# Performance work log

Hardware: AMD Instinct MI355X
Metric: run time of the kernel (lower is better)

The kernel has to match this reference:

```python
import jax, jax.numpy as jnp
import numpy as np

# Model dims (match init_kwargs)
V, D, NH, H, NL = 32000, 512, 8, 2048, 2
B = 8
SOS = 1
EPS = 1e-5  # PyTorch LayerNorm default
TEMP = 0.8


def _pe(length, d):
    # Sinusoidal positional encoding, same math as PositionalEncoding
    pos = jnp.arange(length, dtype=jnp.float32)[:, None]
    div = jnp.exp(jnp.arange(0, d, 2, dtype=jnp.float32) * (-np.log(10000.0) / d))
    pe = jnp.zeros((length, d), dtype=jnp.float32)
    pe = pe.at[:, 0::2].set(jnp.sin(pos * div))
    pe = pe.at[:, 1::2].set(jnp.cos(pos * div))
    return pe


def _ln(x, g, b):
    m = jnp.mean(x, -1, keepdims=True)
    v = jnp.mean((x - m) ** 2, -1, keepdims=True)
    return (x - m) / jnp.sqrt(v + EPS) * g + b


def _mha(q_in, kv_in, in_w, in_b, out_w, out_b, nh, mask):
    # PyTorch nn.MultiheadAttention math (packed in_proj, scale 1/sqrt(head_dim))
    Bq, S, d = q_in.shape
    Sk = kv_in.shape[1]
    hd = d // nh
    wq, wk, wv = jnp.split(in_w, 3, axis=0)
    bq, bk, bv = jnp.split(in_b, 3, axis=0)
    q = (q_in @ wq.T + bq).reshape(Bq, S, nh, hd).transpose(0, 2, 1, 3)
    k = (kv_in @ wk.T + bk).reshape(Bq, Sk, nh, hd).transpose(0, 2, 1, 3)
    v = (kv_in @ wv.T + bv).reshape(Bq, Sk, nh, hd).transpose(0, 2, 1, 3)
    s = jnp.einsum('bhqd,bhkd->bhqk', q, k) / np.sqrt(hd)
    if mask is not None:
        s = s + mask
    p = jax.nn.softmax(s, axis=-1)
    o = jnp.einsum('bhqk,bhkd->bhqd', p, v).transpose(0, 2, 1, 3).reshape(Bq, S, d)
    return o @ out_w.T + out_b


def _forward(memory, embedding,
             sa_in_w, sa_in_b, sa_out_w, sa_out_b,
             ca_in_w, ca_in_b, ca_out_w, ca_out_b,
             ff1_w, ff1_b, ff2_w, ff2_b,
             ln1_g, ln1_b, ln2_g, ln2_b, ln3_g, ln3_b,
             out_w, out_b, max_len):
    L = int(max_len)
    S = L + 1  # padded generated-sequence length (SOS + L tokens)
    pe = _pe(S, D)
    causal = jnp.triu(jnp.full((S, S), -jnp.inf, dtype=jnp.float32), k=1)
    mem = memory[:, None, :]  # (B,1,D), as in forward's unsqueeze(1)
    tokens0 = jnp.zeros((B, S), dtype=jnp.int32).at[:, 0].set(SOS)

    # Each step re-runs the full decoder over the (padded) sequence with a
    # causal mask; due to causality the output at row t equals the original
    # loop's output over the length-(t+1) prefix. Dropout = identity (eval).
    def step(tokens, t):
        x = embedding[tokens] + pe[None, :, :]
        for l in range(NL):
            sa = _mha(x, x, sa_in_w[l], sa_in_b[l], sa_out_w[l], sa_out_b[l], NH, causal)
            x = _ln(x + sa, ln1_g[l], ln1_b[l])
            ca = _mha(x, mem, ca_in_w[l], ca_in_b[l], ca_out_w[l], ca_out_b[l], NH, None)
            x = _ln(x + ca, ln2_g[l], ln2_b[l])
            ff = jax.nn.relu(x @ ff1_w[l].T + ff1_b[l]) @ ff2_w[l].T + ff2_b[l]
            x = _ln(x + ff, ln3_g[l], ln3_b[l])
        h = x[:, t]  # hidden state at current position (B,D)
        logits = h @ out_w.T + out_b  # (B,V)
        nxt = jnp.argmax(logits / TEMP, axis=-1).astype(jnp.int32)  # greedy
        tokens = tokens.at[:, t + 1].set(nxt)
        return tokens, logits

    tokens, logits = jax.lax.scan(step, tokens0, jnp.arange(L))
    return tokens[:, 1:], jnp.transpose(logits, (1, 0, 2))  # (B,L), (B,L,V)


def setup_inputs() -> dict:
    key = jax.random.key(0)
    ks = jax.random.split(key, 16)
    s = 0.02
    n = lambda k, shp: jax.random.normal(k, shp, dtype=jnp.float32) * s
    return {
        'memory': jax.random.normal(ks[0], (B, D), dtype=jnp.float32),
        'embedding': n(ks[1], (V, D)),
        'sa_in_w': n(ks[2], (NL, 3 * D, D)), 'sa_in_b': jnp.zeros((NL, 3 * D)),
        'sa_out_w': n(ks[3], (NL, D, D)), 'sa_out_b': jnp.zeros((NL, D)),
        'ca_in_w': n(ks[4], (NL, 3 * D, D)), 'ca_in_b': jnp.zeros((NL, 3 * D)),
        'ca_out_w': n(ks[5], (NL, D, D)), 'ca_out_b': jnp.zeros((NL, D)),
        'ff1_w': n(ks[6], (NL, H, D)), 'ff1_b': jnp.zeros((NL, H)),
        'ff2_w': n(ks[7], (NL, D, H)), 'ff2_b': jnp.zeros((NL, D)),
        'ln1_g': jnp.ones((NL, D)), 'ln1_b': jnp.zeros((NL, D)),
        'ln2_g': jnp.ones((NL, D)), 'ln2_b': jnp.zeros((NL, D)),
        'ln3_g': jnp.ones((NL, D)), 'ln3_b': jnp.zeros((NL, D)),
        'out_w': n(ks[8], (V, D)), 'out_b': jnp.zeros((V,)),
        'max_len': 48,
    }


def reference(memory, embedding,
              sa_in_w, sa_in_b, sa_out_w, sa_out_b,
              ca_in_w, ca_in_b, ca_out_w, ca_out_b,
              ff1_w, ff1_b, ff2_w, ff2_b,
              ln1_g, ln1_b, ln2_g, ln2_b, ln3_g, ln3_b,
              out_w, out_b, max_len):
    return _forward(memory, embedding,
                    sa_in_w, sa_in_b, sa_out_w, sa_out_b,
                    ca_in_w, ca_in_b, ca_out_w, ca_out_b,
                    ff1_w, ff1_b, ff2_w, ff2_b,
                    ln1_g, ln1_b, ln2_g, ln2_b, ln3_g, ln3_b,
                    out_w, out_b, max_len)
```

## Files before the change

### kernel.cpp

```cpp
#include <hip/hip_runtime.h>
#include <math.h>


#define NBK 64
#define NTH 512
#define NGRP 32

namespace cfg {
constexpr int D  = 512;
constexpr int HF = 2048;
constexpr int V  = 32000;
constexpr int TMAX = 64;
constexpr int VPB  = V / NBK;
constexpr float EPS = 1e-5f;
constexpr float PE_NEG = -0.017988946039015984f;

constexpr size_t O_CAV  = 4096;
constexpr size_t O_CAC  = O_CAV + 2 * 8 * 512;
constexpr size_t O_ATT  = O_CAC + 2 * 8 * 512;
constexpr size_t O_Y1   = O_ATT + 8 * 512;
constexpr size_t O_Y2   = O_Y1  + 8 * 512;
constexpr size_t O_HFF  = O_Y2  + 8 * 512;
constexpr size_t O_CAND = O_HFF + 8 * 2048;
}

typedef float f4v __attribute__((ext_vector_type(4)));

__device__ __forceinline__ float ld_dev(const float* p) {
  return __hip_atomic_load(p, __ATOMIC_RELAXED, __HIP_MEMORY_SCOPE_AGENT);
}
__device__ __forceinline__ void st_dev(float* p, float v) {
  __hip_atomic_store(p, v, __ATOMIC_RELAXED, __HIP_MEMORY_SCOPE_AGENT);
}
union F2U { float2 f; unsigned long long u; };
__device__ __forceinline__ float2 ld_dev2(const float2* p) {
  F2U x; x.u = __hip_atomic_load((const unsigned long long*)p, __ATOMIC_RELAXED, __HIP_MEMORY_SCOPE_AGENT);
  return x.f;
}
__device__ __forceinline__ void st_dev2(float2* p, float2 v) {
  F2U x; x.f = v;
  __hip_atomic_store((unsigned long long*)p, x.u, __ATOMIC_RELAXED, __HIP_MEMORY_SCOPE_AGENT);
}
__device__ __forceinline__ unsigned ld_devu(const unsigned* p) {
  return __hip_atomic_load(p, __ATOMIC_RELAXED, __HIP_MEMORY_SCOPE_AGENT);
}
__device__ __forceinline__ void st_devu(unsigned* p, unsigned v) {
  __hip_atomic_store(p, v, __ATOMIC_RELAXED, __HIP_MEMORY_SCOPE_AGENT);
}

template <typename EPI>
__device__ __forceinline__ void gemv512(const float* __restrict__ W,
                                        const float* __restrict__ bias,
                                        int R, int NW, int bid,
                                        const float* xs, EPI&& epi) {
  const int tid = threadIdx.x;
  const int gl  = tid & 15;
  const int grp = tid >> 4;
  for (int r = grp * NW + bid; r < R; r += NW * NGRP) {
    const f4v* wr = (const f4v*)(W + (size_t)r * cfg::D);
    float acc[8] = {0.f, 0.f, 0.f, 0.f, 0.f, 0.f, 0.f, 0.f};
#pragma unroll
    for (int i = 0; i < 8; ++i) {
      const f4v w = wr[gl + 16 * i];
#pragma unroll
      for (int b = 0; b < 8; ++b) {
        const float4 a = ((const float4*)(xs + b * cfg::D))[gl + 16 * i];
        acc[b] = fmaf(w[0], a.x, acc[b]);
        acc[b] = fmaf(w[1], a.y, acc[b]);
        acc[b] = fmaf(w[2], a.z, acc[b]);
        acc[b] = fmaf(w[3], a.w, acc[b]);
      }
    }
#pragma unroll
    for (int b = 0; b < 8; ++b) {
      float v = acc[b];
      v += __shfl_xor(v, 1);
      v += __shfl_xor(v, 2);
      v += __shfl_xor(v, 4);
      v += __shfl_xor(v, 8);
      acc[b] = v;
    }
    if (gl < 8) {
      float v = acc[gl];
      if (bias) v += bias[r];
      epi(gl, r, v);
    }
  }
}

__launch_bounds__(NTH)
__global__ void decoder_persistent(
    const float* __restrict__ memory, const float* __restrict__ embedding,
    const float* __restrict__ sa_in_w, const float* __restrict__ sa_in_b,
    const float* __restrict__ sa_out_w, const float* __restrict__ sa_out_b,
    const float* __restrict__ ca_in_w, const float* __restrict__ ca_in_b,
    const float* __restrict__ ca_out_w, const float* __restrict__ ca_out_b,
    const float* __restrict__ ff1_w, const float* __restrict__ ff1_b,
    const float* __restrict__ ff2_w, const float* __restrict__ ff2_b,
    const float* __restrict__ ln1_g, const float* __restrict__ ln1_b,
    const float* __restrict__ ln2_g, const float* __restrict__ ln2_b,
    const float* __restrict__ ln3_g, const float* __restrict__ ln3_b,
    const float* __restrict__ out_w, const float* __restrict__ out_b,
    const int* __restrict__ max_len_p,
    float* __restrict__ dout, float* __restrict__ wsf) {
  using namespace cfg;
  __shared__ __align__(16) float xs[8192];
  __shared__ float kch[2][TMAX][64];
  __shared__ float vch[2][TMAX][64];
  __shared__ float ltile[8][VPB + 16];
  __shared__ float q_s[64];
  __shared__ float p_l[64];
  __shared__ float div_ls[256];
  __shared__ float2 redc[64];
  __shared__ float2 gcand[NGRP * 8];
  __shared__ int tok_ls[8];

  const int tid  = threadIdx.x;
  const int w    = tid >> 6;
  const int lane = tid & 63;
  const int col0 = lane * 8;
  const int gl   = tid & 15;
  const int grp  = tid >> 4;
  const int L    = max_len_p[0];
  const int widx = (int)blockIdx.x;
  const int ab = widx >> 3;
  const int ah = widx & 7;

  unsigned* wflag = (unsigned*)wsf;

  float*  cav  = wsf + O_CAV;
  float*  cac  = wsf + O_CAC;
  float*  attb = wsf + O_ATT;
  float*  y1   = wsf + O_Y1;
  float*  y2   = wsf + O_Y2;
  float*  hff  = wsf + O_HFF;
  float2* cand = (float2*)(wsf + O_CAND);
  float*  dlog = dout + (size_t)8 * L;

  unsigned wbarn = 0;

  auto wsync = [&]() {
    __syncthreads();
    ++wbarn;
    if (tid == 0) st_devu(&wflag[widx * 32], wbarn);
    if (w == 0) {
      while (true) {
        const unsigned v = ld_devu(&wflag[lane * 32]);
        if (__ballot(v < wbarn) == 0ull) break;
        __builtin_amdgcn_s_sleep(1);
      }
    }
    __syncthreads();
  };

  auto wave_ln = [&](float (&v)[8], const float* g, const float* bta) {
    float s = 0.f, s2 = 0.f;
#pragma unroll
    for (int j = 0; j < 8; ++j) { s += v[j]; s2 = fmaf(v[j], v[j], s2); }
#pragma unroll
    for (int m = 1; m < 64; m <<= 1) { s += __shfl_xor(s, m); s2 += __shfl_xor(s2, m); }
    const float mean = s * (1.f / 512.f);
    const float var  = s2 * (1.f / 512.f) - mean * mean;
    const float inv  = 1.0f / sqrtf(var + EPS);
    const float4 g0 = ((const float4*)(g + col0))[0], g1 = ((const float4*)(g + col0))[1];
    const float4 b0 = ((const float4*)(bta + col0))[0], b1 = ((const float4*)(bta + col0))[1];
    const float gg[8] = {g0.x, g0.y, g0.z, g0.w, g1.x, g1.y, g1.z, g1.w};
    const float bb[8] = {b0.x, b0.y, b0.z, b0.w, b1.x, b1.y, b1.z, b1.w};
#pragma unroll
    for (int j = 0; j < 8; ++j) v[j] = (v[j] - mean) * inv * gg[j] + bb[j];
  };

  if (tid < 256) div_ls[tid] = expf((float)(2 * tid) * PE_NEG);
  {
    const int gtid = widx * NTH + tid;
    if (gtid < 2 * 8 * 512) {
      const int b = gtid & 7, r = (gtid >> 3) & 511, l = gtid >> 12;
      const float4* a4 = (const float4*)(memory + (size_t)b * 512);
      const float4* w4 = (const float4*)(ca_in_w + ((size_t)l * 1536 + 1024 + r) * 512);
      float s = 0.f;
      for (int i = 0; i < 128; ++i) {
        const float4 a = a4[i], ww = w4[i];
        s = fmaf(a.x, ww.x, s); s = fmaf(a.y, ww.y, s);
        s = fmaf(a.z, ww.z, s); s = fmaf(a.w, ww.w, s);
      }
      st_dev(&cav[((size_t)l * 8 + b) * 512 + r], s + ca_in_b[l * 1536 + 1024 + r]);
    }
  }
  wsync();
  {
    const int gtid = widx * NTH + tid;
    if (gtid < 2 * 8 * 512) {
      const int b = gtid & 7, r = (gtid >> 3) & 511, l = gtid >> 12;
      const float* a = cav + ((size_t)l * 8 + b) * 512;
      const float4* w4 = (const float4*)(ca_out_w + ((size_t)l * 512 + r) * 512);
      float s = 0.f;
      for (int i = 0; i < 128; ++i) {
        const float4 ww = w4[i];
        s = fmaf(ld_dev(a + 4 * i + 0), ww.x, s);
        s = fmaf(ld_dev(a + 4 * i + 1), ww.y, s);
        s = fmaf(ld_dev(a + 4 * i + 2), ww.z, s);
        s = fmaf(ld_dev(a + 4 * i + 3), ww.w, s);
      }
      st_dev(&cac[((size_t)l * 8 + b) * 512 + r], s + ca_out_b[l * 512 + r]);
    }
  }
  wsync();

  float x0r[8];
  float x2r[8];
  if (tid < 8) tok_ls[tid] = 1;
  __syncthreads();

  for (int t = 0; t < L; ++t) {
    for (int l = 0; l < 2; ++l) {
      if (l == 0) {
        const int tok = tok_ls[w];
        const float4* e4 = (const float4*)(embedding + (size_t)tok * 512 + col0);
        const float4 e0 = e4[0], e1 = e4[1];
        float v[8] = {e0.x, e0.y, e0.z, e0.w, e1.x, e1.y, e1.z, e1.w};
#pragma unroll
        for (int j = 0; j < 8; ++j) {
          const int c = col0 + j;
          const float ang = (float)t * div_ls[c >> 1];
          v[j] += (c & 1) ? cosf(ang) : sinf(ang);
          x0r[j] = v[j];
          xs[w * 512 + c] = v[j];
        }
        __syncthreads();
      } else {
        float v[8];
#pragma unroll
        for (int j = 0; j < 8; ++j) v[j] = x2r[j] + ld_dev(y2 + (size_t)w * 512 + col0 + j);
        wave_ln(v, ln3_g, ln3_b);
#pragma unroll
        for (int j = 0; j < 8; ++j) { x0r[j] = v[j]; xs[w * 512 + col0 + j] = v[j]; }
        __syncthreads();
      }

      {
        for (int it = 0; it < 6; ++it) {
          const int rr = grp + 32 * it;
          const int type = rr >> 6, d = rr & 63;
          const int wrow = type * 512 + ah * 64 + d;
          const float4* wr = (const float4*)(sa_in_w + ((size_t)l * 1536 + wrow) * 512);
          const float4* a4 = (const float4*)(xs + (size_t)ab * 512);
          float s = 0.f;
#pragma unroll
          for (int i = 0; i < 8; ++i) {
            const float4 ww = wr[gl + 16 * i], a = a4[gl + 16 * i];
            s = fmaf(ww.x, a.x, s); s = fmaf(ww.y, a.y, s);
            s = fmaf(ww.z, a.z, s); s = fmaf(ww.w, a.w, s);
          }
          s += __shfl_xor(s, 1);
          s += __shfl_xor(s, 2);
          s += __shfl_xor(s, 4);
          s += __shfl_xor(s, 8);
          if (gl == 0) {
            s += sa_in_b[l * 1536 + wrow];
            if (type == 0)      q_s[d] = s;
            else if (type == 1) kch[l][t][d] = s;
            else                vch[l][t][d] = s;
          }
        }
        __syncthreads();
        for (int j = w; j <= t; j += 8) {
          float s = q_s[lane] * kch[l][j][lane];
          s += __shfl_xor(s, 1);
          s += __shfl_xor(s, 2);
          s += __shfl_xor(s, 4);
          s += __shfl_xor(s, 8);
          s += __shfl_xor(s, 16);
          s += __shfl_xor(s, 32);
          if (lane == 0) p_l[j] = s * 0.125f;
        }
        __syncthreads();
        float mx = -3.4e38f;
        for (int j = 0; j <= t; ++j) mx = fmaxf(mx, p_l[j]);
        __syncthreads();
        if (tid <= t) p_l[tid] = expf(p_l[tid] - mx);
        __syncthreads();
        if (w == 0) {
          float den = 0.f, o = 0.f;
          for (int j = 0; j <= t; ++j) {
            const float p = p_l[j];
            den += p;
            o = fmaf(p, vch[l][j][lane], o);
          }
          st_dev(&attb[(size_t)ab * 512 + ah * 64 + lane], o / den);
        }
      }
      wsync();

      for (int j = tid; j < 2048; j += NTH)
        ((float2*)xs)[j] = ld_dev2((const float2*)attb + j);
      __syncthreads();
      gemv512(sa_out_w + (size_t)l * 512 * 512, sa_out_b + l * 512, 512,
              NBK, widx, xs,
              [&](int b, int r, float val) { st_dev(&y1[(size_t)b * 512 + r], val); });
      wsync();

      {
        float v[8];
#pragma unroll
        for (int j = 0; j < 8; ++j) v[j] = x0r[j] + ld_dev(y1 + (size_t)w * 512 + col0 + j);
        wave_ln(v, ln1_g + l * 512, ln1_b + l * 512);
#pragma unroll
        for (int j = 0; j < 8; ++j) v[j] += ld_dev(cac + ((size_t)l * 8 + w) * 512 + col0 + j);
        wave_ln(v, ln2_g + l * 512, ln2_b + l * 512);
#pragma unroll
        for (int j = 0; j < 8; ++j) { x2r[j] = v[j]; xs[w * 512 + col0 + j] = v[j]; }
        __syncthreads();
      }
      gemv512(ff1_w + (size_t)l * HF * 512, ff1_b + l * HF, HF,
              NBK, widx, xs,
              [&](int b, int r, float val) {
                st_dev(&hff[(size_t)b * HF + r], fmaxf(val, 0.f));
              });
      wsync();

      {
        const bool act = (grp < 8);
        const int r = (grp & 7) * 64 + widx;
        float acc[8] = {0.f, 0.f, 0.f, 0.f, 0.f, 0.f, 0.f, 0.f};
        for (int tile = 0; tile < 2; ++tile) {
          __syncthreads();
          for (int j = tid; j < 4096; j += NTH)
            ((float2*)xs)[j] = ld_dev2((const float2*)hff + (size_t)(j >> 9) * 1024 +
                                       tile * 512 + (j & 511));
          __syncthreads();
          if (act) {
            const float4* wr = (const float4*)(ff2_w + ((size_t)l * 512 + r) * HF +
                                               (size_t)tile * 1024);
#pragma unroll
            for (int i = 0; i < 16; ++i) {
              const float4 ww = wr[gl + 16 * i];
#pragma unroll
              for (int b2 = 0; b2 < 8; ++b2) {
                const float4 a = ((const float4*)xs)[b2 * 256 + gl + 16 * i];
                acc[b2] = fmaf(ww.x, a.x, acc[b2]);
                acc[b2] = fmaf(ww.y, a.y, acc[b2]);
                acc[b2] = fmaf(ww.z, a.z, acc[b2]);
                acc[b2] = fmaf(ww.w, a.w, acc[b2]);
              }
            }
          }
        }
        if (act) {
#pragma unroll
          for (int b2 = 0; b2 < 8; ++b2) {
            float v = acc[b2];
            v += __shfl_xor(v, 1);
            v += __shfl_xor(v, 2);
            v += __shfl_xor(v, 4);
            v += __shfl_xor(v, 8);
            acc[b2] = v;
          }
          if (gl < 8) st_dev(&y2[(size_t)gl * 512 + r], acc[gl] + ff2_b[l * 512 + r]);
        }
      }
      wsync();
    }

    {
      float v[8];
#pragma unroll
      for (int j = 0; j < 8; ++j) v[j] = x2r[j] + ld_dev(y2 + (size_t)w * 512 + col0 + j);
      wave_ln(v, ln3_g + 512, ln3_b + 512);
#pragma unroll
      for (int j = 0; j < 8; ++j) xs[w * 512 + col0 + j] = v[j];
      __syncthreads();
    }

    {
      const int rbase = widx * VPB;
      float bestv = -3.4e38f, besti = 0.f;
      for (int it = 0; it < 16; ++it) {
        const int rloc = it * 32 + grp;
        if (rloc < VPB) {
          const f4v* wr = (const f4v*)(out_w + (size_t)(rbase + rloc) * 512);
          float acc[8] = {0.f, 0.f, 0.f, 0.f, 0.f, 0.f, 0.f, 0.f};
#pragma unroll
          for (int i = 0; i < 8; ++i) {
            const f4v ww = wr[gl + 16 * i];
#pragma unroll
            for (int b = 0; b < 8; ++b) {
              const float4 a = ((const float4*)(xs + b * 512))[gl + 16 * i];
              acc[b] = fmaf(ww[0], a.x, acc[b]);
              acc[b] = fmaf(ww[1], a.y, acc[b]);
              acc[b] = fmaf(ww[2], a.z, acc[b]);
              acc[b] = fmaf(ww[3], a.w, acc[b]);
            }
          }
#pragma unroll
          for (int b = 0; b < 8; ++b) {
            float v = acc[b];
            v += __shfl_xor(v, 1);
            v += __shfl_xor(v, 2);
            v += __shfl_xor(v, 4);
            v += __shfl_xor(v, 8);
            acc[b] = v;
          }
          if (gl < 8) {
            const float val = acc[gl] + out_b[rbase + rloc];
            ltile[gl][rloc] = val;
            if (val > bestv) { bestv = val; besti = (float)(rbase + rloc); }
          }
        }
      }
      if (gl < 8) gcand[grp * 8 + gl] = make_float2(bestv, besti);
      __syncthreads();
#pragma unroll
      for (int b = 0; b < 8; ++b) {
        if (tid < VPB)
          __builtin_nontemporal_store(ltile[b][tid],
                                      &dlog[((size_t)b * L + t) * V + rbase + tid]);
      }
      if (tid < 8) {
        float bv = -3.4e38f, bi = 0.f;
        for (int g2 = 0; g2 < NGRP; ++g2) {
          const float2 cv = gcand[g2 * 8 + tid];
          if (cv.x > bv || (cv.x == bv && cv.y < bi)) { bv = cv.x; bi = cv.y; }
        }
        st_dev2(&cand[(size_t)widx * 8 + tid], make_float2(bv, bi));
      }
    }
    wsync();

    {
      if (tid < 64) {
        const int b = tid & 7, j0 = (tid >> 3) << 3;
        float bv = -3.4e38f, bi = 0.f;
#pragma unroll
        for (int jj = 0; jj < 8; ++jj) {
          const float2 cv = ld_dev2(&cand[(size_t)(j0 + jj) * 8 + b]);
          if (cv.x > bv || (cv.x == bv && cv.y < bi)) { bv = cv.x; bi = cv.y; }
        }
        redc[tid] = make_float2(bv, bi);
      }
      __syncthreads();
      if (tid < 8) {
        float bv = -3.4e38f, bi = 0.f;
        for (int c = 0; c < 8; ++c) {
          const float2 cv = redc[c * 8 + tid];
          if (cv.x > bv || (cv.x == bv && cv.y < bi)) { bv = cv.x; bi = cv.y; }
        }
        tok_ls[tid] = (int)bi;
        if (widx == 0) dout[(size_t)tid * L + t] = bi;
      }
      __syncthreads();
    }
  }
}

extern "C" void kernel_launch(void* const* d_in, const int* in_sizes, int n_in,
                              void* d_out, int out_size, void* d_ws, size_t ws_size,
                              hipStream_t stream) {
  (void)in_sizes; (void)n_in; (void)out_size; (void)ws_size;
  hipMemsetAsync(d_ws, 0, 16384, stream);

  const float* memory    = (const float*)d_in[0];
  const float* embedding = (const float*)d_in[1];
  const float* sa_in_w   = (const float*)d_in[2];
  const float* sa_in_b   = (const float*)d_in[3];
  const float* sa_out_w  = (const float*)d_in[4];
  const float* sa_out_b  = (const float*)d_in[5];
  const float* ca_in_w   = (const float*)d_in[6];
  const float* ca_in_b   = (const float*)d_in[7];
  const float* ca_out_w  = (const float*)d_in[8];
  const float* ca_out_b  = (const float*)d_in[9];
  const float* ff1_w     = (const float*)d_in[10];
  const float* ff1_b     = (const float*)d_in[11];
  const float* ff2_w     = (const float*)d_in[12];
  const float* ff2_b     = (const float*)d_in[13];
  const float* ln1_g     = (const float*)d_in[14];
  const float* ln1_b     = (const float*)d_in[15];
  const float* ln2_g     = (const float*)d_in[16];
  const float* ln2_b     = (const float*)d_in[17];
  const float* ln3_g     = (const float*)d_in[18];
  const float* ln3_b     = (const float*)d_in[19];
  const float* out_w     = (const float*)d_in[20];
  const float* out_b     = (const float*)d_in[21];
  const int*   max_len   = (const int*)d_in[22];

  hipLaunchKernelGGL(decoder_persistent, dim3(NBK), dim3(NTH), 0, stream,
                     memory, embedding, sa_in_w, sa_in_b, sa_out_w, sa_out_b,
                     ca_in_w, ca_in_b, ca_out_w, ca_out_b, ff1_w, ff1_b,
                     ff2_w, ff2_b, ln1_g, ln1_b, ln2_g, ln2_b, ln3_g, ln3_b,
                     out_w, out_b, max_len, (float*)d_out, (float*)d_ws);
}
```

Baseline: 5.541 ms.

## Add helper blocks to split vocab projection across 256 workgroups

The grid grows from 64 to 256 blocks. The 64 worker blocks still run the decoder layers. The 192 extra helper blocks wait on a barrier flag, read the final hidden state from a device buffer, and each compute a slice of the 32000-row output projection and argmax. This spreads the large logits GEMV over many more CUs, at the cost of spinning helper blocks and an extra handshake through device-scope flags each step.

```diff
diff --git a/kernel.cpp b/kernel.cpp
--- a/kernel.cpp
+++ b/kernel.cpp
@@ -2,7 +2,8 @@
 #include <math.h>
 
 
-#define NBK 64
+#define NBK 256
+#define NWRK 64
 #define NTH 512
 #define NGRP 32
 
@@ -15,13 +16,14 @@
 constexpr float EPS = 1e-5f;
 constexpr float PE_NEG = -0.017988946039015984f;
 
-constexpr size_t O_CAV  = 4096;
+constexpr size_t O_CAV  = 8192;
 constexpr size_t O_CAC  = O_CAV + 2 * 8 * 512;
 constexpr size_t O_ATT  = O_CAC + 2 * 8 * 512;
 constexpr size_t O_Y1   = O_ATT + 8 * 512;
 constexpr size_t O_Y2   = O_Y1  + 8 * 512;
 constexpr size_t O_HFF  = O_Y2  + 8 * 512;
-constexpr size_t O_CAND = O_HFF + 8 * 2048;
+constexpr size_t O_X3   = O_HFF + 8 * 2048;
+constexpr size_t O_CAND = O_X3  + 8 * 512;
 }
 
 typedef float f4v __attribute__((ext_vector_type(4)));
@@ -107,11 +109,11 @@
   __shared__ __align__(16) float xs[8192];
   __shared__ float kch[2][TMAX][64];
   __shared__ float vch[2][TMAX][64];
-  __shared__ float ltile[8][VPB + 16];
+  __shared__ float ltile[8][VPB + 5];
   __shared__ float q_s[64];
   __shared__ float p_l[64];
   __shared__ float div_ls[256];
-  __shared__ float2 redc[64];
+  __shared__ float2 redc[256];
   __shared__ float2 gcand[NGRP * 8];
   __shared__ int tok_ls[8];
 
@@ -123,10 +125,12 @@
   const int grp  = tid >> 4;
   const int L    = max_len_p[0];
   const int widx = (int)blockIdx.x;
+  const bool isw = widx < NWRK;
   const int ab = widx >> 3;
   const int ah = widx & 7;
 
   unsigned* wflag = (unsigned*)wsf;
+  unsigned* hflag = (unsigned*)wsf + 2048;
 
   float*  cav  = wsf + O_CAV;
   float*  cac  = wsf + O_CAC;
@@ -134,19 +138,119 @@
   float*  y1   = wsf + O_Y1;
   float*  y2   = wsf + O_Y2;
   float*  hff  = wsf + O_HFF;
+  float*  x3d  = wsf + O_X3;
   float2* cand = (float2*)(wsf + O_CAND);
   float*  dlog = dout + (size_t)8 * L;
 
   unsigned wbarn = 0;
+
+  auto logits_slab = [&](int t) {
+    const int rbase = widx * VPB;
+    float bestv = -3.4e38f, besti = 0.f;
+#pragma unroll
+    for (int it = 0; it < 4; ++it) {
+      const int rloc = it * 32 + grp;
+      if (rloc < VPB) {
+        const f4v* wr = (const f4v*)(out_w + (size_t)(rbase + rloc) * 512);
+        float acc[8] = {0.f, 0.f, 0.f, 0.f, 0.f, 0.f, 0.f, 0.f};
+#pragma unroll
+        for (int i = 0; i < 8; ++i) {
+          const f4v ww = wr[gl + 16 * i];
+#pragma unroll
+          for (int b = 0; b < 8; ++b) {
+            const float4 a = ((const float4*)(xs + b * 512))[gl + 16 * i];
+            acc[b] = fmaf(ww[0], a.x, acc[b]);
+            acc[b] = fmaf(ww[1], a.y, acc[b]);
+            acc[b] = fmaf(ww[2], a.z, acc[b]);
+            acc[b] = fmaf(ww[3], a.w, acc[b]);
+          }
+        }
+#pragma unroll
+        for (int b = 0; b < 8; ++b) {
+          float v = acc[b];
+          v += __shfl_xor(v, 1);
+          v += __shfl_xor(v, 2);
+          v += __shfl_xor(v, 4);
+          v += __shfl_xor(v, 8);
+          acc[b] = v;
+        }
+        if (gl < 8) {
+          const float val = acc[gl] + out_b[rbase + rloc];
+          ltile[gl][rloc] = val;
+          if (val > bestv) { bestv = val; besti = (float)(rbase + rloc); }
+        }
+      }
+    }
+    if (gl < 8) gcand[grp * 8 + gl] = make_float2(bestv, besti);
+    __syncthreads();
+#pragma unroll
+    for (int b = 0; b < 8; ++b) {
+      if (tid < VPB)
+        __builtin_nontemporal_store(ltile[b][tid],
+                                    &dlog[((size_t)b * L + t) * V + rbase + tid]);
+    }
+    if (tid < 8) {
+      float bv = -3.4e38f, bi = 0.f;
+      for (int g2 = 0; g2 < NGRP; ++g2) {
+        const float2 cv = gcand[g2 * 8 + tid];
+        if (cv.x > bv || (cv.x == bv && cv.y < bi)) { bv = cv.x; bi = cv.y; }
+      }
+      st_dev2(&cand[(size_t)widx * 8 + tid], make_float2(bv, bi));
+    }
+  };
+
+  if (!isw) {
+    for (int t = 0; t < L; ++t) {
+      const unsigned xgen = 10u * (unsigned)t + 11u;
+      if (w == 0) {
+        while (true) {
+          const unsigned v = ld_devu(&wflag[lane * 32]);
+          if (__ballot(v >= xgen) != 0ull) break;
+          __builtin_amdgcn_s_sleep(2);
+        }
+      }
+      __syncthreads();
+      for (int j = tid; j < 2048; j += NTH)
+        ((float2*)xs)[j] = ld_dev2((const float2*)x3d + j);
+      __syncthreads();
+      logits_slab(t);
+      __syncthreads();
+      if (tid == 0) st_devu(&hflag[(widx - NWRK) * 32], (unsigned)(t + 1));
+    }
+    return;
+  }
+
+  unsigned* myflag = &wflag[widx * 32];
 
   auto wsync = [&]() {
     __syncthreads();
     ++wbarn;
-    if (tid == 0) st_devu(&wflag[widx * 32], wbarn);
+    if (tid == 0) st_devu(myflag, wbarn);
     if (w == 0) {
       while (true) {
         const unsigned v = ld_devu(&wflag[lane * 32]);
         if (__ballot(v < wbarn) == 0ull) break;
+        __builtin_amdgcn_s_sleep(1);
+      }
+    }
+    __syncthreads();
+  };
+
+  auto wsyncE = [&](int t) {
+    __syncthreads();
+    ++wbarn;
+    if (tid == 0) st_devu(myflag, wbarn);
+    if (w == 0) {
+      while (true) {
+        const unsigned v = ld_devu(&wflag[lane * 32]);
+        if (__ballot(v < wbarn) == 0ull) break;
+        __builtin_amdgcn_s_sleep(1);
+      }
+    } else if (w < 4) {
+      const unsigned hexp = (unsigned)(t + 1);
+      while (true) {
+        const unsigned v = ld_devu(&hflag[((w - 1) * 64 + lane) * 32]);
+        if (__ballot(v < hexp) == 0ull) break;
         __builtin_amdgcn_s_sleep(1);
       }
     }
@@ -295,7 +399,7 @@
         ((float2*)xs)[j] = ld_dev2((const float2*)attb + j);
       __syncthreads();
       gemv512(sa_out_w + (size_t)l * 512 * 512, sa_out_b + l * 512, 512,
-              NBK, widx, xs,
+              NWRK, widx, xs,
               [&](int b, int r, float val) { st_dev(&y1[(size_t)b * 512 + r], val); });
       wsync();
 
@@ -312,7 +416,7 @@
         __syncthreads();
       }
       gemv512(ff1_w + (size_t)l * HF * 512, ff1_b + l * HF, HF,
-              NBK, widx, xs,
+              NWRK, widx, xs,
               [&](int b, int r, float val) {
                 st_dev(&hff[(size_t)b * HF + r], fmaxf(val, 0.f));
               });
@@ -371,64 +475,18 @@
       __syncthreads();
     }
 
+    for (int j = tid; j < 2048; j += NTH)
+      st_dev2(&((float2*)x3d)[j], ((const float2*)xs)[j]);
+    __syncthreads();
+    ++wbarn;
+    if (tid == 0) st_devu(myflag, wbarn);
+
+    logits_slab(t);
+    wsyncE(t);
+
     {
-      const int rbase = widx * VPB;
-      float bestv = -3.4e38f, besti = 0.f;
-      for (int it = 0; it < 16; ++it) {
-        const int rloc = it * 32 + grp;
-        if (rloc < VPB) {
-          const f4v* wr = (const f4v*)(out_w + (size_t)(rbase + rloc) * 512);
-          float acc[8] = {0.f, 0.f, 0.f, 0.f, 0.f, 0.f, 0.f, 0.f};
-#pragma unroll
-          for (int i = 0; i < 8; ++i) {
-            const f4v ww = wr[gl + 16 * i];
-#pragma unroll
-            for (int b = 0; b < 8; ++b) {
-              const float4 a = ((const float4*)(xs + b * 512))[gl + 16 * i];
-              acc[b] = fmaf(ww[0], a.x, acc[b]);
-              acc[b] = fmaf(ww[1], a.y, acc[b]);
-              acc[b] = fmaf(ww[2], a.z, acc[b]);
-              acc[b] = fmaf(ww[3], a.w, acc[b]);
-            }
-          }
-#pragma unroll
-          for (int b = 0; b < 8; ++b) {
-            float v = acc[b];
-            v += __shfl_xor(v, 1);
-            v += __shfl_xor(v, 2);
-            v += __shfl_xor(v, 4);
-            v += __shfl_xor(v, 8);
-            acc[b] = v;
-          }
-          if (gl < 8) {
-            const float val = acc[gl] + out_b[rbase + rloc];
-            ltile[gl][rloc] = val;
-            if (val > bestv) { bestv = val; besti = (float)(rbase + rloc); }
-          }
-        }
-      }
-      if (gl < 8) gcand[grp * 8 + gl] = make_float2(bestv, besti);
-      __syncthreads();
-#pragma unroll
-      for (int b = 0; b < 8; ++b) {
-        if (tid < VPB)
-          __builtin_nontemporal_store(ltile[b][tid],
-                                      &dlog[((size_t)b * L + t) * V + rbase + tid]);
-      }
-      if (tid < 8) {
-        float bv = -3.4e38f, bi = 0.f;
-        for (int g2 = 0; g2 < NGRP; ++g2) {
-          const float2 cv = gcand[g2 * 8 + tid];
-          if (cv.x > bv || (cv.x == bv && cv.y < bi)) { bv = cv.x; bi = cv.y; }
-        }
-        st_dev2(&cand[(size_t)widx * 8 + tid], make_float2(bv, bi));
-      }
-    }
-    wsync();
-
-    {
-      if (tid < 64) {
-        const int b = tid & 7, j0 = (tid >> 3) << 3;
+      if (tid < 256) {
+        const int b = tid & 7, j0 = (tid >> 3) * 8;
         float bv = -3.4e38f, bi = 0.f;
 #pragma unroll
         for (int jj = 0; jj < 8; ++jj) {
@@ -440,7 +498,7 @@
       __syncthreads();
       if (tid < 8) {
         float bv = -3.4e38f, bi = 0.f;
-        for (int c = 0; c < 8; ++c) {
+        for (int c = 0; c < 32; ++c) {
           const float2 cv = redc[c * 8 + tid];
           if (cv.x > bv || (cv.x == bv && cv.y < bi)) { bv = cv.x; bi = cv.y; }
         }
@@ -456,7 +514,7 @@
                               void* d_out, int out_size, void* d_ws, size_t ws_size,
                               hipStream_t stream) {
   (void)in_sizes; (void)n_in; (void)out_size; (void)ws_size;
-  hipMemsetAsync(d_ws, 0, 16384, stream);
+  hipMemsetAsync(d_ws, 0, 32768, stream);
 
   const float* memory    = (const float*)d_in[0];
   const float* embedding = (const float*)d_in[1];
```

Result: slower. 6.668 ms (+20.3%).

## Partition decoder layer by (batch, head) per block to drop grid barriers

Applied to the files above, without the earlier changes.

Each of the 64 blocks now owns one (batch, head) pair end to end. The attention output projection and the FFN are computed as per-block partial sums written to global scratch, and they are reduced at the next stage instead of between separate all-block GEMV passes. This removes two grid-wide barriers per layer, and the FFN hidden state stays in shared memory. In exchange, weights are re-read across the eight batch-owning blocks, losing the 8-batch register reuse of the old GEMV, and every consumer now sums eight partials.

```diff
diff --git a/kernel.cpp b/kernel.cpp
--- a/kernel.cpp
+++ b/kernel.cpp
@@ -15,13 +15,12 @@
 constexpr float EPS = 1e-5f;
 constexpr float PE_NEG = -0.017988946039015984f;
 
-constexpr size_t O_CAV  = 4096;
+constexpr size_t O_CAV  = 2048;
 constexpr size_t O_CAC  = O_CAV + 2 * 8 * 512;
-constexpr size_t O_ATT  = O_CAC + 2 * 8 * 512;
-constexpr size_t O_Y1   = O_ATT + 8 * 512;
-constexpr size_t O_Y2   = O_Y1  + 8 * 512;
-constexpr size_t O_HFF  = O_Y2  + 8 * 512;
-constexpr size_t O_CAND = O_HFF + 8 * 2048;
+constexpr size_t O_P1   = O_CAC + 2 * 8 * 512;
+constexpr size_t O_P2   = O_P1  + 64 * 512;
+constexpr size_t O_X2P  = O_P2  + 64 * 512;
+constexpr size_t O_CAND = O_X2P + 8 * 512;
 }
 
 typedef float f4v __attribute__((ext_vector_type(4)));
@@ -46,46 +45,6 @@
 }
 __device__ __forceinline__ void st_devu(unsigned* p, unsigned v) {
   __hip_atomic_store(p, v, __ATOMIC_RELAXED, __HIP_MEMORY_SCOPE_AGENT);
-}
-
-template <typename EPI>
-__device__ __forceinline__ void gemv512(const float* __restrict__ W,
-                                        const float* __restrict__ bias,
-                                        int R, int NW, int bid,
-                                        const float* xs, EPI&& epi) {
-  const int tid = threadIdx.x;
-  const int gl  = tid & 15;
-  const int grp = tid >> 4;
-  for (int r = grp * NW + bid; r < R; r += NW * NGRP) {
-    const f4v* wr = (const f4v*)(W + (size_t)r * cfg::D);
-    float acc[8] = {0.f, 0.f, 0.f, 0.f, 0.f, 0.f, 0.f, 0.f};
-#pragma unroll
-    for (int i = 0; i < 8; ++i) {
-      const f4v w = wr[gl + 16 * i];
-#pragma unroll
-      for (int b = 0; b < 8; ++b) {
-        const float4 a = ((const float4*)(xs + b * cfg::D))[gl + 16 * i];
-        acc[b] = fmaf(w[0], a.x, acc[b]);
-        acc[b] = fmaf(w[1], a.y, acc[b]);
-        acc[b] = fmaf(w[2], a.z, acc[b]);
-        acc[b] = fmaf(w[3], a.w, acc[b]);
-      }
-    }
-#pragma unroll
-    for (int b = 0; b < 8; ++b) {
-      float v = acc[b];
-      v += __shfl_xor(v, 1);
-      v += __shfl_xor(v, 2);
-      v += __shfl_xor(v, 4);
-      v += __shfl_xor(v, 8);
-      acc[b] = v;
-    }
-    if (gl < 8) {
-      float v = acc[gl];
-      if (bias) v += bias[r];
-      epi(gl, r, v);
-    }
-  }
 }
 
 __launch_bounds__(NTH)
@@ -108,6 +67,8 @@
   __shared__ float kch[2][TMAX][64];
   __shared__ float vch[2][TMAX][64];
   __shared__ float ltile[8][VPB + 16];
+  __shared__ __align__(16) float hffs[256];
+  __shared__ __align__(16) float o_s[64];
   __shared__ float q_s[64];
   __shared__ float p_l[64];
   __shared__ float div_ls[256];
@@ -130,10 +91,9 @@
 
   float*  cav  = wsf + O_CAV;
   float*  cac  = wsf + O_CAC;
-  float*  attb = wsf + O_ATT;
-  float*  y1   = wsf + O_Y1;
-  float*  y2   = wsf + O_Y2;
-  float*  hff  = wsf + O_HFF;
+  float*  p1w  = wsf + O_P1;
+  float*  p2w  = wsf + O_P2;
+  float*  x2pb = wsf + O_X2P;
   float2* cand = (float2*)(wsf + O_CAND);
   float*  dlog = dout + (size_t)8 * L;
 
@@ -214,7 +174,7 @@
   for (int t = 0; t < L; ++t) {
     for (int l = 0; l < 2; ++l) {
       if (l == 0) {
-        const int tok = tok_ls[w];
+        const int tok = tok_ls[ab];
         const float4* e4 = (const float4*)(embedding + (size_t)tok * 512 + col0);
         const float4 e0 = e4[0], e1 = e4[1];
         float v[8] = {e0.x, e0.y, e0.z, e0.w, e1.x, e1.y, e1.z, e1.w};
@@ -224,16 +184,32 @@
           const float ang = (float)t * div_ls[c >> 1];
           v[j] += (c & 1) ? cosf(ang) : sinf(ang);
           x0r[j] = v[j];
-          xs[w * 512 + c] = v[j];
+        }
+        if (w == 0) {
+#pragma unroll
+          for (int j = 0; j < 8; ++j) xs[ab * 512 + col0 + j] = v[j];
         }
         __syncthreads();
       } else {
         float v[8];
 #pragma unroll
-        for (int j = 0; j < 8; ++j) v[j] = x2r[j] + ld_dev(y2 + (size_t)w * 512 + col0 + j);
+        for (int jj = 0; jj < 4; ++jj) {
+          float sx = 0.f, sy = 0.f;
+#pragma unroll
+          for (int h = 0; h < 8; ++h) {
+            const float2 p = ld_dev2((const float2*)(p2w + ((size_t)ab * 8 + h) * 512 + col0) + jj);
+            sx += p.x; sy += p.y;
+          }
+          v[2 * jj]     = x2r[2 * jj]     + sx + ff2_b[col0 + 2 * jj];
+          v[2 * jj + 1] = x2r[2 * jj + 1] + sy + ff2_b[col0 + 2 * jj + 1];
+        }
         wave_ln(v, ln3_g, ln3_b);
 #pragma unroll
-        for (int j = 0; j < 8; ++j) { x0r[j] = v[j]; xs[w * 512 + col0 + j] = v[j]; }
+        for (int j = 0; j < 8; ++j) x0r[j] = v[j];
+        if (w == 0) {
+#pragma unroll
+          for (int j = 0; j < 8; ++j) xs[ab * 512 + col0 + j] = v[j];
+        }
         __syncthreads();
       }
 
@@ -286,76 +262,98 @@
             den += p;
             o = fmaf(p, vch[l][j][lane], o);
           }
-          st_dev(&attb[(size_t)ab * 512 + ah * 64 + lane], o / den);
-        }
-      }
-      wsync();
-
-      for (int j = tid; j < 2048; j += NTH)
-        ((float2*)xs)[j] = ld_dev2((const float2*)attb + j);
-      __syncthreads();
-      gemv512(sa_out_w + (size_t)l * 512 * 512, sa_out_b + l * 512, 512,
-              NBK, widx, xs,
-              [&](int b, int r, float val) { st_dev(&y1[(size_t)b * 512 + r], val); });
+          o_s[lane] = o / den;
+        }
+        __syncthreads();
+      }
+
+      {
+        const float4 oo = ((const float4*)o_s)[gl];
+        for (int it = 0; it < 16; ++it) {
+          const int r = it * 32 + grp;
+          const float4 ww = ((const float4*)(sa_out_w + ((size_t)l * 512 + r) * 512 + ah * 64))[gl];
+          float s = ww.x * oo.x;
+          s = fmaf(ww.y, oo.y, s);
+          s = fmaf(ww.z, oo.z, s);
+          s = fmaf(ww.w, oo.w, s);
+          s += __shfl_xor(s, 1);
+          s += __shfl_xor(s, 2);
+          s += __shfl_xor(s, 4);
+          s += __shfl_xor(s, 8);
+          if (gl == 0) st_dev(&p1w[((size_t)ab * 8 + ah) * 512 + r], s);
+        }
+      }
       wsync();
 
       {
         float v[8];
 #pragma unroll
-        for (int j = 0; j < 8; ++j) v[j] = x0r[j] + ld_dev(y1 + (size_t)w * 512 + col0 + j);
+        for (int jj = 0; jj < 4; ++jj) {
+          float sx = 0.f, sy = 0.f;
+#pragma unroll
+          for (int h = 0; h < 8; ++h) {
+            const float2 p = ld_dev2((const float2*)(p1w + ((size_t)ab * 8 + h) * 512 + col0) + jj);
+            sx += p.x; sy += p.y;
+          }
+          v[2 * jj]     = x0r[2 * jj]     + sx + sa_out_b[l * 512 + col0 + 2 * jj];
+          v[2 * jj + 1] = x0r[2 * jj + 1] + sy + sa_out_b[l * 512 + col0 + 2 * jj + 1];
+        }
         wave_ln(v, ln1_g + l * 512, ln1_b + l * 512);
 #pragma unroll
-        for (int j = 0; j < 8; ++j) v[j] += ld_dev(cac + ((size_t)l * 8 + w) * 512 + col0 + j);
+        for (int j = 0; j < 8; ++j) v[j] += ld_dev(cac + ((size_t)l * 8 + ab) * 512 + col0 + j);
         wave_ln(v, ln2_g + l * 512, ln2_b + l * 512);
 #pragma unroll
-        for (int j = 0; j < 8; ++j) { x2r[j] = v[j]; xs[w * 512 + col0 + j] = v[j]; }
-        __syncthreads();
-      }
-      gemv512(ff1_w + (size_t)l * HF * 512, ff1_b + l * HF, HF,
-              NBK, widx, xs,
-              [&](int b, int r, float val) {
-                st_dev(&hff[(size_t)b * HF + r], fmaxf(val, 0.f));
-              });
-      wsync();
+        for (int j = 0; j < 8; ++j) x2r[j] = v[j];
+        if (l == 1 && ah == 0 && w == 0) {
+#pragma unroll
+          for (int j = 0; j < 8; ++j) st_dev(&x2pb[(size_t)ab * 512 + col0 + j], v[j]);
+        }
+        if (w == 0) {
+#pragma unroll
+          for (int j = 0; j < 8; ++j) xs[ab * 512 + col0 + j] = v[j];
+        }
+        __syncthreads();
+      }
 
       {
-        const bool act = (grp < 8);
-        const int r = (grp & 7) * 64 + widx;
-        float acc[8] = {0.f, 0.f, 0.f, 0.f, 0.f, 0.f, 0.f, 0.f};
-        for (int tile = 0; tile < 2; ++tile) {
-          __syncthreads();
-          for (int j = tid; j < 4096; j += NTH)
-            ((float2*)xs)[j] = ld_dev2((const float2*)hff + (size_t)(j >> 9) * 1024 +
-                                       tile * 512 + (j & 511));
-          __syncthreads();
-          if (act) {
-            const float4* wr = (const float4*)(ff2_w + ((size_t)l * 512 + r) * HF +
-                                               (size_t)tile * 1024);
-#pragma unroll
-            for (int i = 0; i < 16; ++i) {
-              const float4 ww = wr[gl + 16 * i];
-#pragma unroll
-              for (int b2 = 0; b2 < 8; ++b2) {
-                const float4 a = ((const float4*)xs)[b2 * 256 + gl + 16 * i];
-                acc[b2] = fmaf(ww.x, a.x, acc[b2]);
-                acc[b2] = fmaf(ww.y, a.y, acc[b2]);
-                acc[b2] = fmaf(ww.z, a.z, acc[b2]);
-                acc[b2] = fmaf(ww.w, a.w, acc[b2]);
-              }
-            }
-          }
-        }
-        if (act) {
-#pragma unroll
-          for (int b2 = 0; b2 < 8; ++b2) {
-            float v = acc[b2];
-            v += __shfl_xor(v, 1);
-            v += __shfl_xor(v, 2);
-            v += __shfl_xor(v, 4);
-            v += __shfl_xor(v, 8);
-            acc[b2] = v;
-          }
-          if (gl < 8) st_dev(&y2[(size_t)gl * 512 + r], acc[gl] + ff2_b[l * 512 + r]);
+        const float4* a4 = (const float4*)(xs + (size_t)ab * 512);
+        for (int it = 0; it < 8; ++it) {
+          const int rl = it * 32 + grp;
+          const int r  = ah * 256 + rl;
+          const float4* wr = (const float4*)(ff1_w + ((size_t)l * HF + r) * 512);
+          float s = 0.f;
+#pragma unroll
+          for (int i = 0; i < 8; ++i) {
+            const float4 ww = wr[gl + 16 * i], a = a4[gl + 16 * i];
+            s = fmaf(ww.x, a.x, s); s = fmaf(ww.y, a.y, s);
+            s = fmaf(ww.z, a.z, s); s = fmaf(ww.w, a.w, s);
+          }
+          s += __shfl_xor(s, 1);
+          s += __shfl_xor(s, 2);
+          s += __shfl_xor(s, 4);
+          s += __shfl_xor(s, 8);
+          if (gl == 0) hffs[rl] = fmaxf(s + ff1_b[l * HF + r], 0.f);
+        }
+        __syncthreads();
+      }
+
+      {
+        for (int it = 0; it < 16; ++it) {
+          const int r = it * 32 + grp;
+          const float4* wr = (const float4*)(ff2_w + ((size_t)l * 512 + r) * HF + ah * 256);
+          float s = 0.f;
+#pragma unroll
+          for (int i = 0; i < 4; ++i) {
+            const float4 ww = wr[gl + 16 * i];
+            const float4 hh = ((const float4*)hffs)[gl + 16 * i];
+            s = fmaf(ww.x, hh.x, s); s = fmaf(ww.y, hh.y, s);
+            s = fmaf(ww.z, hh.z, s); s = fmaf(ww.w, hh.w, s);
+          }
+          s += __shfl_xor(s, 1);
+          s += __shfl_xor(s, 2);
+          s += __shfl_xor(s, 4);
+          s += __shfl_xor(s, 8);
+          if (gl == 0) st_dev(&p2w[((size_t)ab * 8 + ah) * 512 + r], s);
         }
       }
       wsync();
@@ -364,7 +362,17 @@
     {
       float v[8];
 #pragma unroll
-      for (int j = 0; j < 8; ++j) v[j] = x2r[j] + ld_dev(y2 + (size_t)w * 512 + col0 + j);
+      for (int jj = 0; jj < 4; ++jj) {
+        const float2 xp = ld_dev2((const float2*)(x2pb + (size_t)w * 512 + col0) + jj);
+        float sx = 0.f, sy = 0.f;
+#pragma unroll
+        for (int h = 0; h < 8; ++h) {
+          const float2 p = ld_dev2((const float2*)(p2w + ((size_t)w * 8 + h) * 512 + col0) + jj);
+          sx += p.x; sy += p.y;
+        }
+        v[2 * jj]     = xp.x + sx + ff2_b[512 + col0 + 2 * jj];
+        v[2 * jj + 1] = xp.y + sy + ff2_b[512 + col0 + 2 * jj + 1];
+      }
       wave_ln(v, ln3_g + 512, ln3_b + 512);
 #pragma unroll
       for (int j = 0; j < 8; ++j) xs[w * 512 + col0 + j] = v[j];
@@ -456,7 +464,7 @@
                               void* d_out, int out_size, void* d_ws, size_t ws_size,
                               hipStream_t stream) {
   (void)in_sizes; (void)n_in; (void)out_size; (void)ws_size;
-  hipMemsetAsync(d_ws, 0, 16384, stream);
+  hipMemsetAsync(d_ws, 0, 8192, stream);
 
   const float* memory    = (const float*)d_in[0];
   const float* embedding = (const float*)d_in[1];
```

Result: slower. 11.39 ms (+105.5%).

## Split grid barrier into arrive/await and prefetch next stage weights during wait

Applied to the files above, without the earlier changes.

The grid-wide barrier is split into an arrive phase and an await phase. Between them, each thread preloads into registers the first weight row it will use in the next stage (QKV, out-proj, FF1, FF2, or logits), so global weight latency overlaps the barrier spin. The generic gemv512 helper is replaced with inlined per-stage loops that consume the prefetched registers, and the logits weight stream uses nontemporal loads. The cost is 32 extra VGPRs held across barriers, which may add register pressure.

```diff
diff --git a/kernel.cpp b/kernel.cpp
--- a/kernel.cpp
+++ b/kernel.cpp
@@ -46,46 +46,6 @@
 }
 __device__ __forceinline__ void st_devu(unsigned* p, unsigned v) {
   __hip_atomic_store(p, v, __ATOMIC_RELAXED, __HIP_MEMORY_SCOPE_AGENT);
-}
-
-template <typename EPI>
-__device__ __forceinline__ void gemv512(const float* __restrict__ W,
-                                        const float* __restrict__ bias,
-                                        int R, int NW, int bid,
-                                        const float* xs, EPI&& epi) {
-  const int tid = threadIdx.x;
-  const int gl  = tid & 15;
-  const int grp = tid >> 4;
-  for (int r = grp * NW + bid; r < R; r += NW * NGRP) {
-    const f4v* wr = (const f4v*)(W + (size_t)r * cfg::D);
-    float acc[8] = {0.f, 0.f, 0.f, 0.f, 0.f, 0.f, 0.f, 0.f};
-#pragma unroll
-    for (int i = 0; i < 8; ++i) {
-      const f4v w = wr[gl + 16 * i];
-#pragma unroll
-      for (int b = 0; b < 8; ++b) {
-        const float4 a = ((const float4*)(xs + b * cfg::D))[gl + 16 * i];
-        acc[b] = fmaf(w[0], a.x, acc[b]);
-        acc[b] = fmaf(w[1], a.y, acc[b]);
-        acc[b] = fmaf(w[2], a.z, acc[b]);
-        acc[b] = fmaf(w[3], a.w, acc[b]);
-      }
-    }
-#pragma unroll
-    for (int b = 0; b < 8; ++b) {
-      float v = acc[b];
-      v += __shfl_xor(v, 1);
-      v += __shfl_xor(v, 2);
-      v += __shfl_xor(v, 4);
-      v += __shfl_xor(v, 8);
-      acc[b] = v;
-    }
-    if (gl < 8) {
-      float v = acc[gl];
-      if (bias) v += bias[r];
-      epi(gl, r, v);
-    }
-  }
 }
 
 __launch_bounds__(NTH)
@@ -138,11 +98,14 @@
   float*  dlog = dout + (size_t)8 * L;
 
   unsigned wbarn = 0;
-
-  auto wsync = [&]() {
+  float4 pf[8];
+
+  auto arrive = [&]() {
     __syncthreads();
     ++wbarn;
     if (tid == 0) st_devu(&wflag[widx * 32], wbarn);
+  };
+  auto await = [&]() {
     if (w == 0) {
       while (true) {
         const unsigned v = ld_devu(&wflag[lane * 32]);
@@ -151,6 +114,44 @@
       }
     }
     __syncthreads();
+  };
+  auto wsync = [&]() { arrive(); await(); };
+
+  auto pref_qkv = [&](int l) {
+    const float4* wr = (const float4*)(sa_in_w + ((size_t)l * 1536 + ah * 64 + grp) * 512);
+#pragma unroll
+    for (int i = 0; i < 8; ++i) pf[i] = wr[gl + 16 * i];
+    __builtin_amdgcn_sched_barrier(0);
+  };
+  auto pref_op = [&](int l) {
+    const int r = (grp & 7) * 64 + widx;
+    const float4* wr = (const float4*)(sa_out_w + ((size_t)l * 512 + r) * 512);
+#pragma unroll
+    for (int i = 0; i < 8; ++i) pf[i] = wr[gl + 16 * i];
+    __builtin_amdgcn_sched_barrier(0);
+  };
+  auto pref_ff1 = [&](int l) {
+    const int r = grp * 64 + widx;
+    const float4* wr = (const float4*)(ff1_w + ((size_t)l * HF + r) * 512);
+#pragma unroll
+    for (int i = 0; i < 8; ++i) pf[i] = wr[gl + 16 * i];
+    __builtin_amdgcn_sched_barrier(0);
+  };
+  auto pref_ff2 = [&](int l) {
+    const int r = (grp & 7) * 64 + widx;
+    const float4* wr = (const float4*)(ff2_w + ((size_t)l * 512 + r) * HF);
+#pragma unroll
+    for (int i = 0; i < 8; ++i) pf[i] = wr[gl + 16 * i];
+    __builtin_amdgcn_sched_barrier(0);
+  };
+  auto pref_log = [&]() {
+    const f4v* wr = (const f4v*)(out_w + (size_t)(widx * VPB + grp) * 512);
+#pragma unroll
+    for (int i = 0; i < 8; ++i) {
+      const f4v v = __builtin_nontemporal_load(wr + gl + 16 * i);
+      pf[i] = make_float4(v[0], v[1], v[2], v[3]);
+    }
+    __builtin_amdgcn_sched_barrier(0);
   };
 
   auto wave_ln = [&](float (&v)[8], const float* g, const float* bta) {
@@ -211,6 +212,8 @@
   if (tid < 8) tok_ls[tid] = 1;
   __syncthreads();
 
+  pref_qkv(0);
+
   for (int t = 0; t < L; ++t) {
     for (int l = 0; l < 2; ++l) {
       if (l == 0) {
@@ -238,12 +241,26 @@
       }
 
       {
-        for (int it = 0; it < 6; ++it) {
+        const float4* a4 = (const float4*)(xs + (size_t)ab * 512);
+        {
+          float s = 0.f;
+#pragma unroll
+          for (int i = 0; i < 8; ++i) {
+            const float4 ww = pf[i], a = a4[gl + 16 * i];
+            s = fmaf(ww.x, a.x, s); s = fmaf(ww.y, a.y, s);
+            s = fmaf(ww.z, a.z, s); s = fmaf(ww.w, a.w, s);
+          }
+          s += __shfl_xor(s, 1);
+          s += __shfl_xor(s, 2);
+          s += __shfl_xor(s, 4);
+          s += __shfl_xor(s, 8);
+          if (gl == 0) q_s[grp] = s + sa_in_b[l * 1536 + ah * 64 + grp];
+        }
+        for (int it = 1; it < 6; ++it) {
           const int rr = grp + 32 * it;
           const int type = rr >> 6, d = rr & 63;
           const int wrow = type * 512 + ah * 64 + d;
           const float4* wr = (const float4*)(sa_in_w + ((size_t)l * 1536 + wrow) * 512);
-          const float4* a4 = (const float4*)(xs + (size_t)ab * 512);
           float s = 0.f;
 #pragma unroll
           for (int i = 0; i < 8; ++i) {
@@ -289,15 +306,42 @@
           st_dev(&attb[(size_t)ab * 512 + ah * 64 + lane], o / den);
         }
       }
-      wsync();
+      arrive();
+      pref_op(l);
+      await();
 
       for (int j = tid; j < 2048; j += NTH)
         ((float2*)xs)[j] = ld_dev2((const float2*)attb + j);
       __syncthreads();
-      gemv512(sa_out_w + (size_t)l * 512 * 512, sa_out_b + l * 512, 512,
-              NBK, widx, xs,
-              [&](int b, int r, float val) { st_dev(&y1[(size_t)b * 512 + r], val); });
-      wsync();
+      if (grp < 8) {
+        const int r = grp * 64 + widx;
+        float acc[8] = {0.f, 0.f, 0.f, 0.f, 0.f, 0.f, 0.f, 0.f};
+#pragma unroll
+        for (int i = 0; i < 8; ++i) {
+          const float4 ww = pf[i];
+#pragma unroll
+          for (int b = 0; b < 8; ++b) {
+            const float4 a = ((const float4*)(xs + b * 512))[gl + 16 * i];
+            acc[b] = fmaf(ww.x, a.x, acc[b]);
+            acc[b] = fmaf(ww.y, a.y, acc[b]);
+            acc[b] = fmaf(ww.z, a.z, acc[b]);
+            acc[b] = fmaf(ww.w, a.w, acc[b]);
+          }
+        }
+#pragma unroll
+        for (int b = 0; b < 8; ++b) {
+          float v = acc[b];
+          v += __shfl_xor(v, 1);
+          v += __shfl_xor(v, 2);
+          v += __shfl_xor(v, 4);
+          v += __shfl_xor(v, 8);
+          acc[b] = v;
+        }
+        if (gl < 8) st_dev(&y1[(size_t)gl * 512 + r], acc[gl] + sa_out_b[l * 512 + r]);
+      }
+      arrive();
+      pref_ff1(l);
+      await();
 
       {
         float v[8];
@@ -311,12 +355,36 @@
         for (int j = 0; j < 8; ++j) { x2r[j] = v[j]; xs[w * 512 + col0 + j] = v[j]; }
         __syncthreads();
       }
-      gemv512(ff1_w + (size_t)l * HF * 512, ff1_b + l * HF, HF,
-              NBK, widx, xs,
-              [&](int b, int r, float val) {
-                st_dev(&hff[(size_t)b * HF + r], fmaxf(val, 0.f));
-              });
-      wsync();
+      {
+        const int r = grp * 64 + widx;
+        float acc[8] = {0.f, 0.f, 0.f, 0.f, 0.f, 0.f, 0.f, 0.f};
+#pragma unroll
+        for (int i = 0; i < 8; ++i) {
+          const float4 ww = pf[i];
+#pragma unroll
+          for (int b = 0; b < 8; ++b) {
+            const float4 a = ((const float4*)(xs + b * 512))[gl + 16 * i];
+            acc[b] = fmaf(ww.x, a.x, acc[b]);
+            acc[b] = fmaf(ww.y, a.y, acc[b]);
+            acc[b] = fmaf(ww.z, a.z, acc[b]);
+            acc[b] = fmaf(ww.w, a.w, acc[b]);
+          }
+        }
+#pragma unroll
+        for (int b = 0; b < 8; ++b) {
+          float v = acc[b];
+          v += __shfl_xor(v, 1);
+          v += __shfl_xor(v, 2);
+          v += __shfl_xor(v, 4);
+          v += __shfl_xor(v, 8);
+          acc[b] = v;
+        }
+        if (gl < 8)
+          st_dev(&hff[(size_t)gl * HF + r], fmaxf(acc[gl] + ff1_b[l * HF + r], 0.f));
+      }
+      arrive();
+      pref_ff2(l);
+      await();
 
       {
         const bool act = (grp < 8);
@@ -333,7 +401,7 @@
                                                (size_t)tile * 1024);
 #pragma unroll
             for (int i = 0; i < 16; ++i) {
-              const float4 ww = wr[gl + 16 * i];
+              const float4 ww = (tile == 0 && i < 8) ? pf[i] : wr[gl + 16 * i];
 #pragma unroll
               for (int b2 = 0; b2 < 8; ++b2) {
                 const float4 a = ((const float4*)xs)[b2 * 256 + gl + 16 * i];
@@ -358,7 +426,9 @@
           if (gl < 8) st_dev(&y2[(size_t)gl * 512 + r], acc[gl] + ff2_b[l * 512 + r]);
         }
       }
-      wsync();
+      arrive();
+      if (l == 0) pref_qkv(1); else pref_log();
+      await();
     }
 
     {
@@ -374,14 +444,44 @@
     {
       const int rbase = widx * VPB;
       float bestv = -3.4e38f, besti = 0.f;
-      for (int it = 0; it < 16; ++it) {
+      {
+        const int rloc = grp;
+        float acc[8] = {0.f, 0.f, 0.f, 0.f, 0.f, 0.f, 0.f, 0.f};
+#pragma unroll
+        for (int i = 0; i < 8; ++i) {
+          const float4 ww = pf[i];
+#pragma unroll
+          for (int b = 0; b < 8; ++b) {
+            const float4 a = ((const float4*)(xs + b * 512))[gl + 16 * i];
+            acc[b] = fmaf(ww.x, a.x, acc[b]);
+            acc[b] = fmaf(ww.y, a.y, acc[b]);
+            acc[b] = fmaf(ww.z, a.z, acc[b]);
+            acc[b] = fmaf(ww.w, a.w, acc[b]);
+          }
+        }
+#pragma unroll
+        for (int b = 0; b < 8; ++b) {
+          float v = acc[b];
+          v += __shfl_xor(v, 1);
+          v += __shfl_xor(v, 2);
+          v += __shfl_xor(v, 4);
+          v += __shfl_xor(v, 8);
+          acc[b] = v;
+        }
+        if (gl < 8) {
+          const float val = acc[gl] + out_b[rbase + rloc];
+          ltile[gl][rloc] = val;
+          if (val > bestv) { bestv = val; besti = (float)(rbase + rloc); }
+        }
+      }
+      for (int it = 1; it < 16; ++it) {
         const int rloc = it * 32 + grp;
         if (rloc < VPB) {
           const f4v* wr = (const f4v*)(out_w + (size_t)(rbase + rloc) * 512);
           float acc[8] = {0.f, 0.f, 0.f, 0.f, 0.f, 0.f, 0.f, 0.f};
 #pragma unroll
           for (int i = 0; i < 8; ++i) {
-            const f4v ww = wr[gl + 16 * i];
+            const f4v ww = __builtin_nontemporal_load(wr + gl + 16 * i);
 #pragma unroll
             for (int b = 0; b < 8; ++b) {
               const float4 a = ((const float4*)(xs + b * 512))[gl + 16 * i];
@@ -424,7 +524,9 @@
         st_dev2(&cand[(size_t)widx * 8 + tid], make_float2(bv, bi));
       }
     }
-    wsync();
+    arrive();
+    pref_qkv(0);
+    await();
 
     {
       if (tid < 64) {
```

Result: slower. 8.776 ms (+58.4%).
